# Kernel optimization log

Hardware: AMD Instinct MI355X
Metric: run time of the kernel (lower is better)

## Reference

```python
import jax, jax.numpy as jnp
import numpy as np

VOCAB, EMB, HID, T, B = 10000, 1500, 1500, 35, 64
FORGET_BIAS = 1.0

def setup_inputs() -> dict:
    key = jax.random.key(0)
    ks = jax.random.split(key, 8)
    s = 0.02
    return {
        'x': jax.random.randint(ks[0], (T, B), 0, VOCAB),
        'y': jax.random.randint(ks[1], (T, B), 0, VOCAB),
        'embedding': jax.random.normal(ks[2], (VOCAB, EMB), jnp.float32) * s,
        'W0': jax.random.normal(ks[3], (EMB + HID, 4 * HID), jnp.float32) * s,
        'b0': jnp.zeros((4 * HID,), jnp.float32),
        'W1': jax.random.normal(ks[4], (2 * HID, 4 * HID), jnp.float32) * s,
        'b1': jnp.zeros((4 * HID,), jnp.float32),
        'softmax_w': jax.random.normal(ks[5], (HID, VOCAB), jnp.float32) * 0.1,
        'softmax_b': jnp.zeros((VOCAB,), jnp.float32),
    }

def _lstm_step(c, h, x, W, b):
    # TF LSTMCell: z = [x, h] @ W + b; gate order i, j, f, o; forget_bias added to f
    z = jnp.concatenate([x, h], axis=-1) @ W + b
    i, j, f, o = jnp.split(z, 4, axis=-1)
    c_new = c * jax.nn.sigmoid(f + FORGET_BIAS) + jax.nn.sigmoid(i) * jnp.tanh(j)
    h_new = jnp.tanh(c_new) * jax.nn.sigmoid(o)
    return c_new, h_new

def reference(x, y, embedding, W0, b0, W1, b1, softmax_w, softmax_b):
    inputs = embedding[x]  # [T, B, EMB] (time_major)
    zeros = jnp.zeros((B, HID), inputs.dtype)
    init = (zeros, zeros, zeros, zeros)  # (c0, h0, c1, h1)

    def step(carry, xt):
        c0, h0, c1, h1 = carry
        c0, h0 = _lstm_step(c0, h0, xt, W0, b0)
        c1, h1 = _lstm_step(c1, h1, h0, W1, b1)
        return (c0, h0, c1, h1), h1

    _, outputs = jax.lax.scan(step, init, inputs)  # [T, B, HID]
    logits = outputs.reshape(-1, HID) @ softmax_w + softmax_b  # [T*B, VOCAB]
    logp = jax.nn.log_softmax(logits, axis=-1)
    tgt = y.reshape(-1)
    nll = -jnp.take_along_axis(logp, tgt[:, None], axis=-1)[:, 0]
    loss = jnp.sum(nll) / B  # sequence_loss_by_example with unit weights, / batch_size
    return loss
```

## Files before the change

kernel.cpp:

```cpp
#include <hip/hip_runtime.h>
#include <math.h>

#define TT 35
#define BB 64
#define EMB 1500
#define HID 1500
#define VOCAB 10000
#define KT 3072
#define KG 768
#define NCH 24
#define KLP 1504
#define NBLK 158
#define MROWS 2240
#define MPAD 2304
#define LBLK 94
#define FORGET_BIAS 1.0f

typedef __bf16 bf16x8 __attribute__((ext_vector_type(8)));
typedef float f32x4 __attribute__((ext_vector_type(4)));

__device__ __forceinline__ unsigned short f2bf(float f) {
    unsigned int u = __builtin_bit_cast(unsigned int, f);
    u += 0x7fffu + ((u >> 16) & 1u);
    return (unsigned short)(u >> 16);
}
__device__ __forceinline__ float sigmoidf_(float x) { return 1.0f / (1.0f + expf(-x)); }

#define GLOAD_LDS16(gp, lp) __builtin_amdgcn_global_load_lds( \
    (const __attribute__((address_space(1))) void*)(gp),      \
    (__attribute__((address_space(3))) void*)(lp), 16, 0, 0)

__global__ __launch_bounds__(256) void convT(const float* __restrict__ W,
                                             unsigned short* __restrict__ WT,
                                             int K, int N, int KP) {
    __shared__ float tile[32][33];
    int tx = threadIdx.x, ty = threadIdx.y;
    int n0 = blockIdx.x * 32, k0 = blockIdx.y * 32;
#pragma unroll
    for (int i = 0; i < 4; ++i) {
        int k = k0 + ty + 8 * i, n = n0 + tx;
        tile[ty + 8 * i][tx] = (k < K && n < N) ? W[(size_t)k * N + n] : 0.f;
    }
    __syncthreads();
#pragma unroll
    for (int i = 0; i < 4; ++i) {
        int n = n0 + ty + 8 * i, k = k0 + tx;
        if (n < N) WT[(size_t)n * KP + k] = f2bf(tile[tx][ty + 8 * i]);
    }
}

__global__ __launch_bounds__(256) void embed_kernel(const int* __restrict__ x,
                                                    const float* __restrict__ emb,
                                                    unsigned short* __restrict__ A0) {
    int tok = blockIdx.x;
    int v = x[tok];
    const float* src = emb + (size_t)v * EMB;
    unsigned short* dst = A0 + (size_t)tok * KT;
    for (int i = threadIdx.x; i < EMB; i += 256) dst[i] = f2bf(src[i]);
}

__global__ __launch_bounds__(1024) void lstm_pair(
        const unsigned short* __restrict__ A_0, const unsigned short* __restrict__ WT_0,
        const float* __restrict__ bias_0, float* __restrict__ cst_0,
        unsigned short* __restrict__ d1_0, int s1_0, unsigned short* __restrict__ d2_0, int s2_0,
        const unsigned short* __restrict__ A_1, const unsigned short* __restrict__ WT_1,
        const float* __restrict__ bias_1, float* __restrict__ cst_1,
        unsigned short* __restrict__ d1_1, int s1_1, unsigned short* __restrict__ d2_1, int s2_1) {
    __shared__ __align__(16) unsigned char smem[131072];

    const unsigned short* A;  const unsigned short* WT;
    const float* bias;        float* cst;
    unsigned short* d1; int s1; unsigned short* d2; int s2;
    int nb;
    if (blockIdx.x < LBLK) {
        if (!A_0) return;
        A = A_0; WT = WT_0; bias = bias_0; cst = cst_0;
        d1 = d1_0; s1 = s1_0; d2 = d2_0; s2 = s2_0;
        nb = blockIdx.x;
    } else {
        if (!A_1) return;
        A = A_1; WT = WT_1; bias = bias_1; cst = cst_1;
        d1 = d1_1; s1 = s1_1; d2 = d2_1; s2 = s2_1;
        nb = blockIdx.x - LBLK;
    }

    int tid = threadIdx.x;
    int wv = tid >> 6, lane = tid & 63;
    int mt = wv & 3, kg = wv >> 2;
    int quad = lane >> 4, l16 = lane & 15;
    int col = nb * 16 + l16;

    int rr = lane >> 2, p = lane & 3;
    int sp = p ^ (rr & 3);
    int kbase = kg * KG;
    int q0 = mt * 2, q1 = q0 + 1;
    const unsigned short* gp[2];
    int ldsoff[2];
#pragma unroll
    for (int ii = 0; ii < 2; ++ii) {
        int q = ii ? q1 : q0;
        if (q < 4) {
            gp[ii] = A + (size_t)(16 * q + rr) * KT + kbase + sp * 8;
        } else {
            int g = q - 4;
            int ci = nb * 16 + rr; if (ci > HID - 1) ci = HID - 1;
            gp[ii] = WT + (size_t)(g * HID + ci) * KT + kbase + sp * 8;
        }
        ldsoff[ii] = ((q >> 2) * 4 + kg) * 4096 + (q & 3) * 1024;
    }

    int swz = (quad ^ (l16 & 3)) * 16;
    int aoff = (0 * 4 + kg) * 4096 + (mt * 16 + l16) * 64 + swz;
    int boff = (1 * 4 + kg) * 4096 + l16 * 64 + swz;

    f32x4 acc0 = {0.f,0.f,0.f,0.f}, acc1 = acc0, acc2 = acc0, acc3 = acc0;

#pragma unroll
    for (int ci = 0; ci < 3; ++ci) {
        GLOAD_LDS16(gp[0] + ci * 32, smem + ci * 32768 + ldsoff[0]);
        GLOAD_LDS16(gp[1] + ci * 32, smem + ci * 32768 + ldsoff[1]);
    }

    for (int c = 0; c < NCH; ++c) {
        asm volatile("s_waitcnt vmcnt(4)" ::: "memory");
        __builtin_amdgcn_sched_barrier(0);
        __builtin_amdgcn_s_barrier();
        int cs = (c + 3 < NCH) ? (c + 3) : (NCH - 1);
        int bs_ = (c + 3) & 3;
        GLOAD_LDS16(gp[0] + cs * 32, smem + bs_ * 32768 + ldsoff[0]);
        GLOAD_LDS16(gp[1] + cs * 32, smem + bs_ * 32768 + ldsoff[1]);
        const unsigned char* base = smem + (c & 3) * 32768;
        bf16x8 a  = *(const bf16x8*)(base + aoff);
        bf16x8 b0 = *(const bf16x8*)(base + boff);
        bf16x8 b1 = *(const bf16x8*)(base + boff + 1024);
        bf16x8 b2 = *(const bf16x8*)(base + boff + 2048);
        bf16x8 b3 = *(const bf16x8*)(base + boff + 3072);
        __builtin_amdgcn_s_setprio(1);
        acc0 = __builtin_amdgcn_mfma_f32_16x16x32_bf16(a, b0, acc0, 0, 0, 0);
        acc1 = __builtin_amdgcn_mfma_f32_16x16x32_bf16(a, b1, acc1, 0, 0, 0);
        acc2 = __builtin_amdgcn_mfma_f32_16x16x32_bf16(a, b2, acc2, 0, 0, 0);
        acc3 = __builtin_amdgcn_mfma_f32_16x16x32_bf16(a, b3, acc3, 0, 0, 0);
        __builtin_amdgcn_s_setprio(0);
    }
    asm volatile("s_waitcnt vmcnt(0)" ::: "memory");
    __builtin_amdgcn_sched_barrier(0);
    __syncthreads();

    float* red = (float*)smem;
    if (kg > 0) {
        int w = (kg - 1) * 4 + mt;
#pragma unroll
        for (int r = 0; r < 4; ++r) {
            red[(w * 64 + lane) * 16 + r]      = acc0[r];
            red[(w * 64 + lane) * 16 + 4 + r]  = acc1[r];
            red[(w * 64 + lane) * 16 + 8 + r]  = acc2[r];
            red[(w * 64 + lane) * 16 + 12 + r] = acc3[r];
        }
    }
    __syncthreads();
    if (kg == 0) {
#pragma unroll
        for (int k2 = 0; k2 < 3; ++k2) {
            int w = k2 * 4 + mt;
#pragma unroll
            for (int r = 0; r < 4; ++r) {
                acc0[r] += red[(w * 64 + lane) * 16 + r];
                acc1[r] += red[(w * 64 + lane) * 16 + 4 + r];
                acc2[r] += red[(w * 64 + lane) * 16 + 8 + r];
                acc3[r] += red[(w * 64 + lane) * 16 + 12 + r];
            }
        }
        if (col < HID) {
            float bi = bias[col], bj = bias[HID + col];
            float bf_ = bias[2 * HID + col], bo = bias[3 * HID + col];
#pragma unroll
            for (int r = 0; r < 4; ++r) {
                int row = mt * 16 + quad * 4 + r;
                float zi = acc0[r] + bi;
                float zj = acc1[r] + bj;
                float zf = acc2[r] + bf_;
                float zo = acc3[r] + bo;
                int ci = row * HID + col;
                float cn = cst[ci] * sigmoidf_(zf + FORGET_BIAS) + sigmoidf_(zi) * tanhf(zj);
                float hn = tanhf(cn) * sigmoidf_(zo);
                cst[ci] = cn;
                unsigned short hb = f2bf(hn);
                d1[(size_t)row * s1 + col] = hb;
                if (d2) d2[(size_t)row * s2 + col] = hb;
            }
        }
    }
}

__global__ __launch_bounds__(256) void logits_fold(const unsigned short* __restrict__ A,
                                                   const unsigned short* __restrict__ WT,
                                                   const float* __restrict__ sb,
                                                   const int* __restrict__ y,
                                                   float2* __restrict__ partials,
                                                   float* __restrict__ tgtlog) {
    __shared__ __align__(16) unsigned char smem[32768];

    const int NWG = 79 * 18;
    const int NX = 8;
    const int q = NWG / NX, r = NWG % NX;
    int orig = blockIdx.x + 79 * blockIdx.y;
    int xcd = orig % NX, idx = orig / NX;
    int wgid = (xcd < r ? xcd * (q + 1) : r * (q + 1) + (xcd - r) * q) + idx;
    int bn = wgid % 79, mb = wgid / 79;
    int n0 = bn * 128;

    int tid = threadIdx.x;
    int wv = tid >> 6, lane = tid & 63;
    int wr = wv >> 1, wc = wv & 1;
    int quad = lane >> 4, l16 = lane & 15;

    int rr = lane >> 2;
    int ks = (lane & 3) ^ (rr & 3);
    const unsigned short* gA[2]; const unsigned short* gB[2];
    int ldsA[2], ldsB[2];
#pragma unroll
    for (int i = 0; i < 2; ++i) {
        int r16 = wv * 2 + i;
        int ra = mb * 128 + r16 * 16 + rr;
        gA[i] = A + (size_t)ra * KLP + ks * 8;
        ldsA[i] = r16 * 1024;
        int rb = n0 + r16 * 16 + rr;
        if (rb > VOCAB - 1) rb = VOCAB - 1;
        gB[i] = WT + (size_t)rb * KLP + ks * 8;
        ldsB[i] = 8192 + r16 * 1024;
    }

    int sw16 = (quad ^ (l16 & 3)) * 16;
    int aoff[4], boff[4];
#pragma unroll
    for (int f = 0; f < 4; ++f) {
        aoff[f] = (wr * 64 + f * 16 + l16) * 64 + sw16;
        boff[f] = 8192 + (wc * 64 + f * 16 + l16) * 64 + sw16;
    }

    f32x4 acc[4][4];
#pragma unroll
    for (int i = 0; i < 4; ++i)
#pragma unroll
        for (int j = 0; j < 4; ++j) acc[i][j] = (f32x4){0.f, 0.f, 0.f, 0.f};

#pragma unroll
    for (int i = 0; i < 2; ++i) {
        GLOAD_LDS16(gA[i], smem + ldsA[i]);
        GLOAD_LDS16(gB[i], smem + ldsB[i]);
    }
    __syncthreads();

    for (int c = 0; c < KLP / 32; ++c) {
        int buf = c & 1;
        if (c + 1 < KLP / 32) {
            int ob = (buf ^ 1) * 16384;
#pragma unroll
            for (int i = 0; i < 2; ++i) {
                GLOAD_LDS16(gA[i] + (c + 1) * 32, smem + ob + ldsA[i]);
                GLOAD_LDS16(gB[i] + (c + 1) * 32, smem + ob + ldsB[i]);
            }
        }
        const unsigned char* base = smem + buf * 16384;
        bf16x8 a[4], b[4];
#pragma unroll
        for (int f = 0; f < 4; ++f) {
            a[f] = *(const bf16x8*)(base + aoff[f]);
            b[f] = *(const bf16x8*)(base + boff[f]);
        }
#pragma unroll
        for (int ar = 0; ar < 4; ++ar)
#pragma unroll
            for (int cb = 0; cb < 4; ++cb)
                acc[ar][cb] = __builtin_amdgcn_mfma_f32_16x16x32_bf16(a[ar], b[cb], acc[ar][cb], 0, 0, 0);
        __syncthreads();
    }

    int colv[4]; float bs[4];
#pragma unroll
    for (int cb = 0; cb < 4; ++cb) {
        int c = n0 + wc * 64 + cb * 16 + l16;
        colv[cb] = c;
        int cc = (c < VOCAB) ? c : (VOCAB - 1);
        bs[cb] = sb[cc];
    }
    int nb2 = bn * 2 + wc;
#pragma unroll
    for (int ar = 0; ar < 4; ++ar) {
#pragma unroll
        for (int r2 = 0; r2 < 4; ++r2) {
            float v0 = acc[ar][0][r2] + bs[0];
            float v1 = acc[ar][1][r2] + bs[1];
            float v2 = acc[ar][2][r2] + bs[2];
            float v3 = acc[ar][3][r2] + bs[3];
            if (colv[0] >= VOCAB) v0 = -1e30f;
            if (colv[1] >= VOCAB) v1 = -1e30f;
            if (colv[2] >= VOCAB) v2 = -1e30f;
            if (colv[3] >= VOCAB) v3 = -1e30f;
            int row = mb * 128 + wr * 64 + ar * 16 + quad * 4 + r2;
            int t = y[row < MROWS ? row : 0];
            float tv = -1e30f;
            if (colv[0] == t) tv = v0;
            if (colv[1] == t) tv = v1;
            if (colv[2] == t) tv = v2;
            if (colv[3] == t) tv = v3;
            float mx = fmaxf(fmaxf(v0, v1), fmaxf(v2, v3));
#pragma unroll
            for (int d = 1; d < 16; d <<= 1) mx = fmaxf(mx, __shfl_xor(mx, d, 64));
            float sum = expf(v0 - mx) + expf(v1 - mx) + expf(v2 - mx) + expf(v3 - mx);
#pragma unroll
            for (int d = 1; d < 16; d <<= 1) sum += __shfl_xor(sum, d, 64);
#pragma unroll
            for (int d = 1; d < 16; d <<= 1) tv = fmaxf(tv, __shfl_xor(tv, d, 64));
            if (l16 == 0 && row < MROWS) {
                partials[(size_t)row * NBLK + nb2] = make_float2(mx, sum);
                if (tv > -5e29f) tgtlog[row] = tv;
            }
        }
    }
}

__global__ __launch_bounds__(64) void nll_reduce(const float2* __restrict__ partials,
                                                 const float* __restrict__ tgtlog,
                                                 float* __restrict__ nll) {
    int row = blockIdx.x;
    int lane = threadIdx.x;
    float2 loc[3];
    int cnt = 0;
    float m = -1e30f;
    for (int i = lane; i < NBLK; i += 64) {
        float2 p = partials[(size_t)row * NBLK + i];
        loc[cnt++] = p;
        m = fmaxf(m, p.x);
    }
#pragma unroll
    for (int d = 1; d < 64; d <<= 1) m = fmaxf(m, __shfl_xor(m, d, 64));
    float s = 0.f;
    for (int j = 0; j < cnt; ++j) s += loc[j].y * expf(loc[j].x - m);
#pragma unroll
    for (int d = 1; d < 64; d <<= 1) s += __shfl_xor(s, d, 64);
    if (lane == 0) nll[row] = -(tgtlog[row] - m - logf(s));
}

__global__ __launch_bounds__(256) void loss_kernel(const float* __restrict__ nll,
                                                   float* __restrict__ out) {
    __shared__ float red[256];
    int tid = threadIdx.x;
    float s = 0.f;
    for (int i = tid; i < TT * BB; i += 256) s += nll[i];
    red[tid] = s; __syncthreads();
    for (int st = 128; st > 0; st >>= 1) { if (tid < st) red[tid] += red[tid + st]; __syncthreads(); }
    if (tid == 0) out[0] = red[0] / (float)BB;
}

extern "C" void kernel_launch(void* const* d_in, const int* in_sizes, int n_in,
                              void* d_out, int out_size, void* d_ws, size_t ws_size,
                              hipStream_t stream) {
    const int*   x   = (const int*)d_in[0];
    const int*   y   = (const int*)d_in[1];
    const float* emb = (const float*)d_in[2];
    const float* W0  = (const float*)d_in[3];
    const float* b0  = (const float*)d_in[4];
    const float* W1  = (const float*)d_in[5];
    const float* b1  = (const float*)d_in[6];
    const float* sw  = (const float*)d_in[7];
    const float* sb  = (const float*)d_in[8];
    float* out = (float*)d_out;

    char* p = (char*)d_ws;
    unsigned short* A0   = (unsigned short*)p; p += (size_t)TT * BB * KT * 2;
    unsigned short* A1   = (unsigned short*)p; p += (size_t)2 * BB * KT * 2;
    unsigned short* outs = (unsigned short*)p; p += (size_t)MPAD * KLP * 2;
    float* c0 = (float*)p; p += (size_t)BB * HID * 4;
    float* c1 = (float*)p; p += (size_t)BB * HID * 4;
    size_t zero_bytes = (size_t)(p - (char*)d_ws);
    unsigned short* WbT0 = (unsigned short*)p; p += (size_t)6000 * KT * 2;
    unsigned short* WbT1 = (unsigned short*)p; p += (size_t)6000 * KT * 2;
    unsigned short* swT  = (unsigned short*)p; p += (size_t)VOCAB * KLP * 2;
    float2* partials = (float2*)p; p += (size_t)TT * BB * NBLK * 8;
    float* tgtlog = (float*)p; p += (size_t)TT * BB * 4;
    float* nll    = (float*)p;

    hipMemsetAsync(d_ws, 0, zero_bytes, stream);

    dim3 cblk(32, 8);
    convT<<<dim3(188, 96), cblk, 0, stream>>>(W0, WbT0, 3000, 6000, KT);
    convT<<<dim3(188, 96), cblk, 0, stream>>>(W1, WbT1, 3000, 6000, KT);
    convT<<<dim3(313, 47), cblk, 0, stream>>>(sw, swT, HID, VOCAB, KLP);

    embed_kernel<<<TT * BB, 256, 0, stream>>>(x, emb, A0);

    for (int k = 0; k <= TT; ++k) {
        const unsigned short* A0t = (k < TT) ? A0 + (size_t)k * BB * KT : nullptr;
        unsigned short* d1_0 = A1 + (size_t)(k & 1) * BB * KT;
        unsigned short* d2_0 = (k < TT - 1) ? (A0 + (size_t)(k + 1) * BB * KT + EMB) : nullptr;

        const unsigned short* A1t = (k >= 1) ? A1 + (size_t)((k - 1) & 1) * BB * KT : nullptr;
        unsigned short* d1_1 = A1 + (size_t)(k & 1) * BB * KT + HID;
        unsigned short* d2_1 = (k >= 1) ? outs + (size_t)(k - 1) * BB * KLP : nullptr;

        lstm_pair<<<188, 1024, 0, stream>>>(A0t, WbT0, b0, c0, d1_0, KT, d2_0, KT,
                                            A1t, WbT1, b1, c1, d1_1, KT, d2_1, KLP);
    }

    logits_fold<<<dim3(79, 18), 256, 0, stream>>>(outs, swT, sb, y, partials, tgtlog);
    nll_reduce<<<TT * BB, 64, 0, stream>>>(partials, tgtlog, nll);
    loss_kernel<<<1, 256, 0, stream>>>(nll, out);
}
```

Measured before the change: 1.255 ms.

## Hoist layer-0 input projection out of recurrence into one batched GEMM

Splits W0 into input and hidden halves and precomputes the embedding-times-Wx projection for all timesteps in a single large GEMM (zx_gemm) before the recurrent loop. Each layer-0 step then does only the hidden K=1536 reduction and adds the precomputed bf16 Zx in the epilogue, halving the sequential layer-0 work. This adds an extra kernel, a Zx buffer round trip, and extra bf16 rounding of the input projection. The logits_fold block-to-XCD remapping is also changed to a 1D grid with an explicit assignment.

```diff
diff --git a/kernel.cpp b/kernel.cpp
--- a/kernel.cpp
+++ b/kernel.cpp
@@ -9,11 +9,15 @@
 #define KT 3072
 #define KG 768
 #define NCH 24
+#define KH 1536
+#define KGH 384
+#define NCHH 12
 #define KLP 1504
 #define NBLK 158
 #define MROWS 2240
 #define MPAD 2304
 #define LBLK 94
+#define ZXN 6000
 #define FORGET_BIAS 1.0f
 
 typedef __bf16 bf16x8 __attribute__((ext_vector_type(8)));
@@ -23,6 +27,10 @@
     unsigned int u = __builtin_bit_cast(unsigned int, f);
     u += 0x7fffu + ((u >> 16) & 1u);
     return (unsigned short)(u >> 16);
+}
+__device__ __forceinline__ float bf2f(unsigned short u) {
+    unsigned int v = ((unsigned int)u) << 16;
+    return __builtin_bit_cast(float, v);
 }
 __device__ __forceinline__ float sigmoidf_(float x) { return 1.0f / (1.0f + expf(-x)); }
 
@@ -51,18 +59,104 @@
 
 __global__ __launch_bounds__(256) void embed_kernel(const int* __restrict__ x,
                                                     const float* __restrict__ emb,
-                                                    unsigned short* __restrict__ A0) {
+                                                    unsigned short* __restrict__ Ae) {
     int tok = blockIdx.x;
     int v = x[tok];
     const float* src = emb + (size_t)v * EMB;
-    unsigned short* dst = A0 + (size_t)tok * KT;
+    unsigned short* dst = Ae + (size_t)tok * KH;
     for (int i = threadIdx.x; i < EMB; i += 256) dst[i] = f2bf(src[i]);
+}
+
+__global__ __launch_bounds__(256) void zx_gemm(const unsigned short* __restrict__ A,
+                                               const unsigned short* __restrict__ WT,
+                                               unsigned short* __restrict__ Zx) {
+    __shared__ __align__(16) unsigned char smem[32768];
+    int orig = blockIdx.x;
+    int xcd = orig & 7, j = orig >> 3;
+    int mb, bn;
+    if (xcd < 7) { bn = xcd * 6 + j % 6; mb = j / 6; }
+    else { if (j >= 90) return; bn = 42 + j % 5; mb = j / 5; }
+    int n0 = bn * 128;
+
+    int tid = threadIdx.x;
+    int wv = tid >> 6, lane = tid & 63;
+    int wr = wv >> 1, wc = wv & 1;
+    int quad = lane >> 4, l16 = lane & 15;
+    int rr = lane >> 2;
+    int ks = (lane & 3) ^ (rr & 3);
+    const unsigned short* gA[2]; const unsigned short* gB[2];
+    int ldsA[2], ldsB[2];
+#pragma unroll
+    for (int i = 0; i < 2; ++i) {
+        int r16 = wv * 2 + i;
+        int ra = mb * 128 + r16 * 16 + rr;
+        gA[i] = A + (size_t)ra * KH + ks * 8;
+        ldsA[i] = r16 * 1024;
+        int rb = n0 + r16 * 16 + rr;
+        if (rb > 5999) rb = 5999;
+        gB[i] = WT + (size_t)rb * KH + ks * 8;
+        ldsB[i] = 8192 + r16 * 1024;
+    }
+    int sw16 = (quad ^ (l16 & 3)) * 16;
+    int aoff[4], boff[4];
+#pragma unroll
+    for (int f = 0; f < 4; ++f) {
+        aoff[f] = (wr * 64 + f * 16 + l16) * 64 + sw16;
+        boff[f] = 8192 + (wc * 64 + f * 16 + l16) * 64 + sw16;
+    }
+    f32x4 acc[4][4];
+#pragma unroll
+    for (int i = 0; i < 4; ++i)
+#pragma unroll
+        for (int jj = 0; jj < 4; ++jj) acc[i][jj] = (f32x4){0.f, 0.f, 0.f, 0.f};
+
+#pragma unroll
+    for (int i = 0; i < 2; ++i) {
+        GLOAD_LDS16(gA[i], smem + ldsA[i]);
+        GLOAD_LDS16(gB[i], smem + ldsB[i]);
+    }
+    __syncthreads();
+    for (int c = 0; c < KH / 32; ++c) {
+        int buf = c & 1;
+        if (c + 1 < KH / 32) {
+            int ob = (buf ^ 1) * 16384;
+#pragma unroll
+            for (int i = 0; i < 2; ++i) {
+                GLOAD_LDS16(gA[i] + (c + 1) * 32, smem + ob + ldsA[i]);
+                GLOAD_LDS16(gB[i] + (c + 1) * 32, smem + ob + ldsB[i]);
+            }
+        }
+        const unsigned char* base = smem + buf * 16384;
+        bf16x8 a[4], b[4];
+#pragma unroll
+        for (int f = 0; f < 4; ++f) {
+            a[f] = *(const bf16x8*)(base + aoff[f]);
+            b[f] = *(const bf16x8*)(base + boff[f]);
+        }
+#pragma unroll
+        for (int ar = 0; ar < 4; ++ar)
+#pragma unroll
+            for (int cb = 0; cb < 4; ++cb)
+                acc[ar][cb] = __builtin_amdgcn_mfma_f32_16x16x32_bf16(a[ar], b[cb], acc[ar][cb], 0, 0, 0);
+        __syncthreads();
+    }
+#pragma unroll
+    for (int ar = 0; ar < 4; ++ar)
+#pragma unroll
+        for (int cb = 0; cb < 4; ++cb)
+#pragma unroll
+            for (int r2 = 0; r2 < 4; ++r2) {
+                int row = mb * 128 + wr * 64 + ar * 16 + quad * 4 + r2;
+                int col = n0 + wc * 64 + cb * 16 + l16;
+                if (col < ZXN) Zx[(size_t)row * ZXN + col] = f2bf(acc[ar][cb][r2]);
+            }
 }
 
 __global__ __launch_bounds__(1024) void lstm_pair(
         const unsigned short* __restrict__ A_0, const unsigned short* __restrict__ WT_0,
         const float* __restrict__ bias_0, float* __restrict__ cst_0,
         unsigned short* __restrict__ d1_0, int s1_0, unsigned short* __restrict__ d2_0, int s2_0,
+        const unsigned short* __restrict__ zx_0,
         const unsigned short* __restrict__ A_1, const unsigned short* __restrict__ WT_1,
         const float* __restrict__ bias_1, float* __restrict__ cst_1,
         unsigned short* __restrict__ d1_1, int s1_1, unsigned short* __restrict__ d2_1, int s2_1) {
@@ -71,16 +165,19 @@
     const unsigned short* A;  const unsigned short* WT;
     const float* bias;        float* cst;
     unsigned short* d1; int s1; unsigned short* d2; int s2;
-    int nb;
+    const unsigned short* zx;
+    int nb, kstr, kgK, nch;
     if (blockIdx.x < LBLK) {
         if (!A_0) return;
         A = A_0; WT = WT_0; bias = bias_0; cst = cst_0;
         d1 = d1_0; s1 = s1_0; d2 = d2_0; s2 = s2_0;
+        zx = zx_0; kstr = KH; kgK = KGH; nch = NCHH;
         nb = blockIdx.x;
     } else {
         if (!A_1) return;
         A = A_1; WT = WT_1; bias = bias_1; cst = cst_1;
         d1 = d1_1; s1 = s1_1; d2 = d2_1; s2 = s2_1;
+        zx = nullptr; kstr = KT; kgK = KG; nch = NCH;
         nb = blockIdx.x - LBLK;
     }
 
@@ -92,7 +189,7 @@
 
     int rr = lane >> 2, p = lane & 3;
     int sp = p ^ (rr & 3);
-    int kbase = kg * KG;
+    int kbase = kg * kgK;
     int q0 = mt * 2, q1 = q0 + 1;
     const unsigned short* gp[2];
     int ldsoff[2];
@@ -100,11 +197,11 @@
     for (int ii = 0; ii < 2; ++ii) {
         int q = ii ? q1 : q0;
         if (q < 4) {
-            gp[ii] = A + (size_t)(16 * q + rr) * KT + kbase + sp * 8;
+            gp[ii] = A + (size_t)(16 * q + rr) * kstr + kbase + sp * 8;
         } else {
             int g = q - 4;
             int ci = nb * 16 + rr; if (ci > HID - 1) ci = HID - 1;
-            gp[ii] = WT + (size_t)(g * HID + ci) * KT + kbase + sp * 8;
+            gp[ii] = WT + (size_t)(g * HID + ci) * kstr + kbase + sp * 8;
         }
         ldsoff[ii] = ((q >> 2) * 4 + kg) * 4096 + (q & 3) * 1024;
     }
@@ -121,11 +218,11 @@
         GLOAD_LDS16(gp[1] + ci * 32, smem + ci * 32768 + ldsoff[1]);
     }
 
-    for (int c = 0; c < NCH; ++c) {
+    for (int c = 0; c < nch; ++c) {
         asm volatile("s_waitcnt vmcnt(4)" ::: "memory");
         __builtin_amdgcn_sched_barrier(0);
         __builtin_amdgcn_s_barrier();
-        int cs = (c + 3 < NCH) ? (c + 3) : (NCH - 1);
+        int cs = (c + 3 < nch) ? (c + 3) : (nch - 1);
         int bs_ = (c + 3) & 3;
         GLOAD_LDS16(gp[0] + cs * 32, smem + bs_ * 32768 + ldsoff[0]);
         GLOAD_LDS16(gp[1] + cs * 32, smem + bs_ * 32768 + ldsoff[1]);
@@ -180,6 +277,13 @@
                 float zj = acc1[r] + bj;
                 float zf = acc2[r] + bf_;
                 float zo = acc3[r] + bo;
+                if (zx) {
+                    const unsigned short* zr = zx + (size_t)row * ZXN;
+                    zi += bf2f(zr[col]);
+                    zj += bf2f(zr[HID + col]);
+                    zf += bf2f(zr[2 * HID + col]);
+                    zo += bf2f(zr[3 * HID + col]);
+                }
                 int ci = row * HID + col;
                 float cn = cst[ci] * sigmoidf_(zf + FORGET_BIAS) + sigmoidf_(zi) * tanhf(zj);
                 float hn = tanhf(cn) * sigmoidf_(zo);
@@ -200,13 +304,11 @@
                                                    float* __restrict__ tgtlog) {
     __shared__ __align__(16) unsigned char smem[32768];
 
-    const int NWG = 79 * 18;
-    const int NX = 8;
-    const int q = NWG / NX, r = NWG % NX;
-    int orig = blockIdx.x + 79 * blockIdx.y;
-    int xcd = orig % NX, idx = orig / NX;
-    int wgid = (xcd < r ? xcd * (q + 1) : r * (q + 1) + (xcd - r) * q) + idx;
-    int bn = wgid % 79, mb = wgid / 79;
+    int orig = blockIdx.x;
+    int xcd = orig & 7, j = orig >> 3;
+    int mb, bn;
+    if (xcd < 7) { bn = xcd * 10 + j % 10; mb = j / 10; }
+    else { if (j >= 162) return; bn = 70 + j % 9; mb = j / 9; }
     int n0 = bn * 128;
 
     int tid = threadIdx.x;
@@ -242,7 +344,7 @@
 #pragma unroll
     for (int i = 0; i < 4; ++i)
 #pragma unroll
-        for (int j = 0; j < 4; ++j) acc[i][j] = (f32x4){0.f, 0.f, 0.f, 0.f};
+        for (int jj = 0; jj < 4; ++jj) acc[i][jj] = (f32x4){0.f, 0.f, 0.f, 0.f};
 
 #pragma unroll
     for (int i = 0; i < 2; ++i) {
@@ -336,7 +438,7 @@
 #pragma unroll
     for (int d = 1; d < 64; d <<= 1) m = fmaxf(m, __shfl_xor(m, d, 64));
     float s = 0.f;
-    for (int j = 0; j < cnt; ++j) s += loc[j].y * expf(loc[j].x - m);
+    for (int jj = 0; jj < cnt; ++jj) s += loc[jj].y * expf(loc[jj].x - m);
 #pragma unroll
     for (int d = 1; d < 64; d <<= 1) s += __shfl_xor(s, d, 64);
     if (lane == 0) nll[row] = -(tgtlog[row] - m - logf(s));
@@ -368,13 +470,16 @@
     float* out = (float*)d_out;
 
     char* p = (char*)d_ws;
-    unsigned short* A0   = (unsigned short*)p; p += (size_t)TT * BB * KT * 2;
+    unsigned short* Ae   = (unsigned short*)p; p += (size_t)MPAD * KH * 2;
     unsigned short* A1   = (unsigned short*)p; p += (size_t)2 * BB * KT * 2;
+    unsigned short* H0   = (unsigned short*)p; p += (size_t)2 * BB * KH * 2;
     unsigned short* outs = (unsigned short*)p; p += (size_t)MPAD * KLP * 2;
     float* c0 = (float*)p; p += (size_t)BB * HID * 4;
     float* c1 = (float*)p; p += (size_t)BB * HID * 4;
     size_t zero_bytes = (size_t)(p - (char*)d_ws);
-    unsigned short* WbT0 = (unsigned short*)p; p += (size_t)6000 * KT * 2;
+    unsigned short* Zx   = (unsigned short*)p; p += (size_t)MPAD * ZXN * 2;
+    unsigned short* WxT0 = (unsigned short*)p; p += (size_t)6000 * KH * 2;
+    unsigned short* WhT0 = (unsigned short*)p; p += (size_t)6000 * KH * 2;
     unsigned short* WbT1 = (unsigned short*)p; p += (size_t)6000 * KT * 2;
     unsigned short* swT  = (unsigned short*)p; p += (size_t)VOCAB * KLP * 2;
     float2* partials = (float2*)p; p += (size_t)TT * BB * NBLK * 8;
@@ -384,26 +489,29 @@
     hipMemsetAsync(d_ws, 0, zero_bytes, stream);
 
     dim3 cblk(32, 8);
-    convT<<<dim3(188, 96), cblk, 0, stream>>>(W0, WbT0, 3000, 6000, KT);
+    convT<<<dim3(188, 48), cblk, 0, stream>>>(W0, WxT0, 1500, 6000, KH);
+    convT<<<dim3(188, 48), cblk, 0, stream>>>(W0 + (size_t)1500 * 6000, WhT0, 1500, 6000, KH);
     convT<<<dim3(188, 96), cblk, 0, stream>>>(W1, WbT1, 3000, 6000, KT);
     convT<<<dim3(313, 47), cblk, 0, stream>>>(sw, swT, HID, VOCAB, KLP);
 
-    embed_kernel<<<TT * BB, 256, 0, stream>>>(x, emb, A0);
+    embed_kernel<<<TT * BB, 256, 0, stream>>>(x, emb, Ae);
+    zx_gemm<<<864, 256, 0, stream>>>(Ae, WxT0, Zx);
 
     for (int k = 0; k <= TT; ++k) {
-        const unsigned short* A0t = (k < TT) ? A0 + (size_t)k * BB * KT : nullptr;
+        const unsigned short* A0t = (k < TT) ? H0 + (size_t)((k - 1) & 1) * BB * KH : nullptr;
         unsigned short* d1_0 = A1 + (size_t)(k & 1) * BB * KT;
-        unsigned short* d2_0 = (k < TT - 1) ? (A0 + (size_t)(k + 1) * BB * KT + EMB) : nullptr;
+        unsigned short* d2_0 = H0 + (size_t)(k & 1) * BB * KH;
+        const unsigned short* zx0 = Zx + (size_t)k * BB * ZXN;
 
         const unsigned short* A1t = (k >= 1) ? A1 + (size_t)((k - 1) & 1) * BB * KT : nullptr;
         unsigned short* d1_1 = A1 + (size_t)(k & 1) * BB * KT + HID;
         unsigned short* d2_1 = (k >= 1) ? outs + (size_t)(k - 1) * BB * KLP : nullptr;
 
-        lstm_pair<<<188, 1024, 0, stream>>>(A0t, WbT0, b0, c0, d1_0, KT, d2_0, KT,
+        lstm_pair<<<188, 1024, 0, stream>>>(A0t, WhT0, b0, c0, d1_0, KT, d2_0, KH, zx0,
                                             A1t, WbT1, b1, c1, d1_1, KT, d2_1, KLP);
     }
 
-    logits_fold<<<dim3(79, 18), 256, 0, stream>>>(outs, swT, sb, y, partials, tgtlog);
+    logits_fold<<<1440, 256, 0, stream>>>(outs, swT, sb, y, partials, tgtlog);
     nll_reduce<<<TT * BB, 64, 0, stream>>>(partials, tgtlog, nll);
     loss_kernel<<<1, 256, 0, stream>>>(nll, out);
 }
```

After: 1.303 ms. 3.9% more time.

## Deepen logits GEMM pipeline, remap blocks per XCD, strengthen LDS swizzle

Applied to the files above, without the earlier changes.

The logits GEMM moves from a double-buffered to a 4-stage LDS ring with loads issued three chunks ahead. It uses a waitcnt plus a raw barrier in place of the two syncthreads per iteration, and raises wave priority around the MFMA block. Workgroups are remapped so each XCD owns a contiguous band of vocabulary columns, which is meant to improve L2 reuse of the softmax weights. Both the LSTM and logits kernels get an extra XOR term in the LDS swizzle to cut bank conflicts. The cost is 64KB of LDS per block, which may lower occupancy, and a 1D launch with early-exit blocks on the last XCD.

```diff
diff --git a/kernel.cpp b/kernel.cpp
--- a/kernel.cpp
+++ b/kernel.cpp
@@ -91,7 +91,7 @@
     int col = nb * 16 + l16;
 
     int rr = lane >> 2, p = lane & 3;
-    int sp = p ^ (rr & 3);
+    int sp = p ^ (rr & 3) ^ ((rr >> 2) & 3);
     int kbase = kg * KG;
     int q0 = mt * 2, q1 = q0 + 1;
     const unsigned short* gp[2];
@@ -109,7 +109,7 @@
         ldsoff[ii] = ((q >> 2) * 4 + kg) * 4096 + (q & 3) * 1024;
     }
 
-    int swz = (quad ^ (l16 & 3)) * 16;
+    int swz = (quad ^ (l16 & 3) ^ ((l16 >> 2) & 3)) * 16;
     int aoff = (0 * 4 + kg) * 4096 + (mt * 16 + l16) * 64 + swz;
     int boff = (1 * 4 + kg) * 4096 + l16 * 64 + swz;
 
@@ -198,15 +198,13 @@
                                                    const int* __restrict__ y,
                                                    float2* __restrict__ partials,
                                                    float* __restrict__ tgtlog) {
-    __shared__ __align__(16) unsigned char smem[32768];
-
-    const int NWG = 79 * 18;
-    const int NX = 8;
-    const int q = NWG / NX, r = NWG % NX;
-    int orig = blockIdx.x + 79 * blockIdx.y;
-    int xcd = orig % NX, idx = orig / NX;
-    int wgid = (xcd < r ? xcd * (q + 1) : r * (q + 1) + (xcd - r) * q) + idx;
-    int bn = wgid % 79, mb = wgid / 79;
+    __shared__ __align__(16) unsigned char smem[65536];
+
+    int orig = blockIdx.x;
+    int xcd = orig & 7, j = orig >> 3;
+    int mb, bn;
+    if (xcd < 7) { bn = xcd * 10 + j % 10; mb = j / 10; }
+    else { if (j >= 162) return; bn = 70 + j % 9; mb = j / 9; }
     int n0 = bn * 128;
 
     int tid = threadIdx.x;
@@ -215,7 +213,7 @@
     int quad = lane >> 4, l16 = lane & 15;
 
     int rr = lane >> 2;
-    int ks = (lane & 3) ^ (rr & 3);
+    int ks = (lane & 3) ^ (rr & 3) ^ ((rr >> 2) & 3);
     const unsigned short* gA[2]; const unsigned short* gB[2];
     int ldsA[2], ldsB[2];
 #pragma unroll
@@ -230,7 +228,7 @@
         ldsB[i] = 8192 + r16 * 1024;
     }
 
-    int sw16 = (quad ^ (l16 & 3)) * 16;
+    int sw16 = (quad ^ (l16 & 3) ^ ((l16 >> 2) & 3)) * 16;
     int aoff[4], boff[4];
 #pragma unroll
     for (int f = 0; f < 4; ++f) {
@@ -242,47 +240,53 @@
 #pragma unroll
     for (int i = 0; i < 4; ++i)
 #pragma unroll
-        for (int j = 0; j < 4; ++j) acc[i][j] = (f32x4){0.f, 0.f, 0.f, 0.f};
-
-#pragma unroll
-    for (int i = 0; i < 2; ++i) {
-        GLOAD_LDS16(gA[i], smem + ldsA[i]);
-        GLOAD_LDS16(gB[i], smem + ldsB[i]);
-    }
-    __syncthreads();
-
-    for (int c = 0; c < KLP / 32; ++c) {
-        int buf = c & 1;
-        if (c + 1 < KLP / 32) {
-            int ob = (buf ^ 1) * 16384;
-#pragma unroll
-            for (int i = 0; i < 2; ++i) {
-                GLOAD_LDS16(gA[i] + (c + 1) * 32, smem + ob + ldsA[i]);
-                GLOAD_LDS16(gB[i] + (c + 1) * 32, smem + ob + ldsB[i]);
-            }
-        }
-        const unsigned char* base = smem + buf * 16384;
+        for (int jj = 0; jj < 4; ++jj) acc[i][jj] = (f32x4){0.f, 0.f, 0.f, 0.f};
+
+    const int NCHL = KLP / 32;
+#pragma unroll
+    for (int ci = 0; ci < 3; ++ci)
+#pragma unroll
+        for (int i = 0; i < 2; ++i) {
+            GLOAD_LDS16(gA[i] + ci * 32, smem + ci * 16384 + ldsA[i]);
+            GLOAD_LDS16(gB[i] + ci * 32, smem + ci * 16384 + ldsB[i]);
+        }
+    for (int c = 0; c < NCHL; ++c) {
+        asm volatile("s_waitcnt vmcnt(8)" ::: "memory");
+        __builtin_amdgcn_sched_barrier(0);
+        __builtin_amdgcn_s_barrier();
+        int cs = (c + 3 < NCHL) ? (c + 3) : (NCHL - 1);
+        int ob = ((c + 3) & 3) * 16384;
+#pragma unroll
+        for (int i = 0; i < 2; ++i) {
+            GLOAD_LDS16(gA[i] + cs * 32, smem + ob + ldsA[i]);
+            GLOAD_LDS16(gB[i] + cs * 32, smem + ob + ldsB[i]);
+        }
+        const unsigned char* base = smem + (c & 3) * 16384;
         bf16x8 a[4], b[4];
 #pragma unroll
         for (int f = 0; f < 4; ++f) {
             a[f] = *(const bf16x8*)(base + aoff[f]);
             b[f] = *(const bf16x8*)(base + boff[f]);
         }
+        __builtin_amdgcn_s_setprio(1);
 #pragma unroll
         for (int ar = 0; ar < 4; ++ar)
 #pragma unroll
-            for (int cb = 0; cb < 4; ++cb)
-                acc[ar][cb] = __builtin_amdgcn_mfma_f32_16x16x32_bf16(a[ar], b[cb], acc[ar][cb], 0, 0, 0);
-        __syncthreads();
-    }
+            for (int cbv = 0; cbv < 4; ++cbv)
+                acc[ar][cbv] = __builtin_amdgcn_mfma_f32_16x16x32_bf16(a[ar], b[cbv], acc[ar][cbv], 0, 0, 0);
+        __builtin_amdgcn_s_setprio(0);
+    }
+    asm volatile("s_waitcnt vmcnt(0)" ::: "memory");
+    __builtin_amdgcn_sched_barrier(0);
+    __syncthreads();
 
     int colv[4]; float bs[4];
 #pragma unroll
-    for (int cb = 0; cb < 4; ++cb) {
-        int c = n0 + wc * 64 + cb * 16 + l16;
-        colv[cb] = c;
+    for (int cbv = 0; cbv < 4; ++cbv) {
+        int c = n0 + wc * 64 + cbv * 16 + l16;
+        colv[cbv] = c;
         int cc = (c < VOCAB) ? c : (VOCAB - 1);
-        bs[cb] = sb[cc];
+        bs[cbv] = sb[cc];
     }
     int nb2 = bn * 2 + wc;
 #pragma unroll
@@ -336,7 +340,7 @@
 #pragma unroll
     for (int d = 1; d < 64; d <<= 1) m = fmaxf(m, __shfl_xor(m, d, 64));
     float s = 0.f;
-    for (int j = 0; j < cnt; ++j) s += loc[j].y * expf(loc[j].x - m);
+    for (int jj = 0; jj < cnt; ++jj) s += loc[jj].y * expf(loc[jj].x - m);
 #pragma unroll
     for (int d = 1; d < 64; d <<= 1) s += __shfl_xor(s, d, 64);
     if (lane == 0) nll[row] = -(tgtlog[row] - m - logf(s));
@@ -403,7 +407,7 @@
                                             A1t, WbT1, b1, c1, d1_1, KT, d2_1, KLP);
     }
 
-    logits_fold<<<dim3(79, 18), 256, 0, stream>>>(outs, swT, sb, y, partials, tgtlog);
+    logits_fold<<<1440, 256, 0, stream>>>(outs, swT, sb, y, partials, tgtlog);
     nll_reduce<<<TT * BB, 64, 0, stream>>>(partials, tgtlog, nll);
     loss_kernel<<<1, 256, 0, stream>>>(nll, out);
 }
```

New measurement: 1.261 ms. No clear change (+0.5%).

## Overlap logits tiles with LSTM recurrence and strengthen LDS swizzle

Applied to the files above, without the earlier changes.

Each recurrent lstm_pair launch now carries up to 48 extra blocks that compute logits/softmax tiles for output rows already produced, which fills idle CUs during the latency-bound recurrence. The remaining tiles run in a reduced logits_fold launch afterward. The LSTM LDS swizzle also gains an extra XOR term to cut bank conflicts. Trade-offs: the extra blocks reserve 128KB of LDS while using only 256 of 1024 threads, and they may contend with the critical-path LSTM blocks. The logits_fold XCD-aware tile remapping is also dropped.

```diff
diff --git a/kernel.cpp b/kernel.cpp
--- a/kernel.cpp
+++ b/kernel.cpp
@@ -14,6 +14,7 @@
 #define MROWS 2240
 #define MPAD 2304
 #define LBLK 94
+#define NTILE 1422
 #define FORGET_BIAS 1.0f
 
 typedef __bf16 bf16x8 __attribute__((ext_vector_type(8)));
@@ -59,14 +60,142 @@
     for (int i = threadIdx.x; i < EMB; i += 256) dst[i] = f2bf(src[i]);
 }
 
+__device__ __forceinline__ void logits_tile_body(
+        int tile, const unsigned short* __restrict__ A,
+        const unsigned short* __restrict__ WT,
+        const float* __restrict__ sb, const int* __restrict__ y,
+        float2* __restrict__ partials, float* __restrict__ tgtlog,
+        unsigned char* smem, int tid) {
+    int mb = tile / 79, bn = tile % 79;
+    int n0 = bn * 128;
+    int wv = tid >> 6, lane = tid & 63;
+    int wr = wv >> 1, wc = wv & 1;
+    int quad = lane >> 4, l16 = lane & 15;
+
+    int rr = lane >> 2;
+    int ks = (lane & 3) ^ (rr & 3);
+    const unsigned short* gA[2]; const unsigned short* gB[2];
+    int ldsA[2], ldsB[2];
+#pragma unroll
+    for (int i = 0; i < 2; ++i) {
+        int r16 = wv * 2 + i;
+        int ra = mb * 128 + r16 * 16 + rr;
+        gA[i] = A + (size_t)ra * KLP + ks * 8;
+        ldsA[i] = r16 * 1024;
+        int rb = n0 + r16 * 16 + rr;
+        if (rb > VOCAB - 1) rb = VOCAB - 1;
+        gB[i] = WT + (size_t)rb * KLP + ks * 8;
+        ldsB[i] = 8192 + r16 * 1024;
+    }
+
+    int sw16 = (quad ^ (l16 & 3)) * 16;
+    int aoff[4], boff[4];
+#pragma unroll
+    for (int f = 0; f < 4; ++f) {
+        aoff[f] = (wr * 64 + f * 16 + l16) * 64 + sw16;
+        boff[f] = 8192 + (wc * 64 + f * 16 + l16) * 64 + sw16;
+    }
+
+    f32x4 acc[4][4];
+#pragma unroll
+    for (int i = 0; i < 4; ++i)
+#pragma unroll
+        for (int jj = 0; jj < 4; ++jj) acc[i][jj] = (f32x4){0.f, 0.f, 0.f, 0.f};
+
+#pragma unroll
+    for (int i = 0; i < 2; ++i) {
+        GLOAD_LDS16(gA[i], smem + ldsA[i]);
+        GLOAD_LDS16(gB[i], smem + ldsB[i]);
+    }
+    __syncthreads();
+
+    for (int c = 0; c < KLP / 32; ++c) {
+        int buf = c & 1;
+        if (c + 1 < KLP / 32) {
+            int ob = (buf ^ 1) * 16384;
+#pragma unroll
+            for (int i = 0; i < 2; ++i) {
+                GLOAD_LDS16(gA[i] + (c + 1) * 32, smem + ob + ldsA[i]);
+                GLOAD_LDS16(gB[i] + (c + 1) * 32, smem + ob + ldsB[i]);
+            }
+        }
+        const unsigned char* base = smem + buf * 16384;
+        bf16x8 a[4], b[4];
+#pragma unroll
+        for (int f = 0; f < 4; ++f) {
+            a[f] = *(const bf16x8*)(base + aoff[f]);
+            b[f] = *(const bf16x8*)(base + boff[f]);
+        }
+#pragma unroll
+        for (int ar = 0; ar < 4; ++ar)
+#pragma unroll
+            for (int cbv = 0; cbv < 4; ++cbv)
+                acc[ar][cbv] = __builtin_amdgcn_mfma_f32_16x16x32_bf16(a[ar], b[cbv], acc[ar][cbv], 0, 0, 0);
+        __syncthreads();
+    }
+
+    int colv[4]; float bs[4];
+#pragma unroll
+    for (int cbv = 0; cbv < 4; ++cbv) {
+        int c = n0 + wc * 64 + cbv * 16 + l16;
+        colv[cbv] = c;
+        int cc = (c < VOCAB) ? c : (VOCAB - 1);
+        bs[cbv] = sb[cc];
+    }
+    int nb2 = bn * 2 + wc;
+#pragma unroll
+    for (int ar = 0; ar < 4; ++ar) {
+#pragma unroll
+        for (int r2 = 0; r2 < 4; ++r2) {
+            float v0 = acc[ar][0][r2] + bs[0];
+            float v1 = acc[ar][1][r2] + bs[1];
+            float v2 = acc[ar][2][r2] + bs[2];
+            float v3 = acc[ar][3][r2] + bs[3];
+            if (colv[0] >= VOCAB) v0 = -1e30f;
+            if (colv[1] >= VOCAB) v1 = -1e30f;
+            if (colv[2] >= VOCAB) v2 = -1e30f;
+            if (colv[3] >= VOCAB) v3 = -1e30f;
+            int row = mb * 128 + wr * 64 + ar * 16 + quad * 4 + r2;
+            int t = y[row < MROWS ? row : 0];
+            float tv = -1e30f;
+            if (colv[0] == t) tv = v0;
+            if (colv[1] == t) tv = v1;
+            if (colv[2] == t) tv = v2;
+            if (colv[3] == t) tv = v3;
+            float mx = fmaxf(fmaxf(v0, v1), fmaxf(v2, v3));
+#pragma unroll
+            for (int d = 1; d < 16; d <<= 1) mx = fmaxf(mx, __shfl_xor(mx, d, 64));
+            float sum = expf(v0 - mx) + expf(v1 - mx) + expf(v2 - mx) + expf(v3 - mx);
+#pragma unroll
+            for (int d = 1; d < 16; d <<= 1) sum += __shfl_xor(sum, d, 64);
+#pragma unroll
+            for (int d = 1; d < 16; d <<= 1) tv = fmaxf(tv, __shfl_xor(tv, d, 64));
+            if (l16 == 0 && row < MROWS) {
+                partials[(size_t)row * NBLK + nb2] = make_float2(mx, sum);
+                if (tv > -5e29f) tgtlog[row] = tv;
+            }
+        }
+    }
+}
+
 __global__ __launch_bounds__(1024) void lstm_pair(
         const unsigned short* __restrict__ A_0, const unsigned short* __restrict__ WT_0,
         const float* __restrict__ bias_0, float* __restrict__ cst_0,
         unsigned short* __restrict__ d1_0, int s1_0, unsigned short* __restrict__ d2_0, int s2_0,
         const unsigned short* __restrict__ A_1, const unsigned short* __restrict__ WT_1,
         const float* __restrict__ bias_1, float* __restrict__ cst_1,
-        unsigned short* __restrict__ d1_1, int s1_1, unsigned short* __restrict__ d2_1, int s2_1) {
+        unsigned short* __restrict__ d1_1, int s1_1, unsigned short* __restrict__ d2_1, int s2_1,
+        const unsigned short* __restrict__ outsA, const unsigned short* __restrict__ swT,
+        const float* __restrict__ sb, const int* __restrict__ y,
+        float2* __restrict__ partials, float* __restrict__ tgtlog, int tile0) {
     __shared__ __align__(16) unsigned char smem[131072];
+
+    if (blockIdx.x >= 2 * LBLK) {
+        if (threadIdx.x >= 256) return;
+        logits_tile_body(tile0 + (int)blockIdx.x - 2 * LBLK, outsA, swT, sb, y,
+                         partials, tgtlog, smem, (int)threadIdx.x);
+        return;
+    }
 
     const unsigned short* A;  const unsigned short* WT;
     const float* bias;        float* cst;
@@ -91,7 +220,7 @@
     int col = nb * 16 + l16;
 
     int rr = lane >> 2, p = lane & 3;
-    int sp = p ^ (rr & 3);
+    int sp = p ^ (rr & 3) ^ ((rr >> 2) & 3);
     int kbase = kg * KG;
     int q0 = mt * 2, q1 = q0 + 1;
     const unsigned short* gp[2];
@@ -109,7 +238,7 @@
         ldsoff[ii] = ((q >> 2) * 4 + kg) * 4096 + (q & 3) * 1024;
     }
 
-    int swz = (quad ^ (l16 & 3)) * 16;
+    int swz = (quad ^ (l16 & 3) ^ ((l16 >> 2) & 3)) * 16;
     int aoff = (0 * 4 + kg) * 4096 + (mt * 16 + l16) * 64 + swz;
     int boff = (1 * 4 + kg) * 4096 + l16 * 64 + swz;
 
@@ -197,127 +326,10 @@
                                                    const float* __restrict__ sb,
                                                    const int* __restrict__ y,
                                                    float2* __restrict__ partials,
-                                                   float* __restrict__ tgtlog) {
+                                                   float* __restrict__ tgtlog, int tile0) {
     __shared__ __align__(16) unsigned char smem[32768];
-
-    const int NWG = 79 * 18;
-    const int NX = 8;
-    const int q = NWG / NX, r = NWG % NX;
-    int orig = blockIdx.x + 79 * blockIdx.y;
-    int xcd = orig % NX, idx = orig / NX;
-    int wgid = (xcd < r ? xcd * (q + 1) : r * (q + 1) + (xcd - r) * q) + idx;
-    int bn = wgid % 79, mb = wgid / 79;
-    int n0 = bn * 128;
-
-    int tid = threadIdx.x;
-    int wv = tid >> 6, lane = tid & 63;
-    int wr = wv >> 1, wc = wv & 1;
-    int quad = lane >> 4, l16 = lane & 15;
-
-    int rr = lane >> 2;
-    int ks = (lane & 3) ^ (rr & 3);
-    const unsigned short* gA[2]; const unsigned short* gB[2];
-    int ldsA[2], ldsB[2];
-#pragma unroll
-    for (int i = 0; i < 2; ++i) {
-        int r16 = wv * 2 + i;
-        int ra = mb * 128 + r16 * 16 + rr;
-        gA[i] = A + (size_t)ra * KLP + ks * 8;
-        ldsA[i] = r16 * 1024;
-        int rb = n0 + r16 * 16 + rr;
-        if (rb > VOCAB - 1) rb = VOCAB - 1;
-        gB[i] = WT + (size_t)rb * KLP + ks * 8;
-        ldsB[i] = 8192 + r16 * 1024;
-    }
-
-    int sw16 = (quad ^ (l16 & 3)) * 16;
-    int aoff[4], boff[4];
-#pragma unroll
-    for (int f = 0; f < 4; ++f) {
-        aoff[f] = (wr * 64 + f * 16 + l16) * 64 + sw16;
-        boff[f] = 8192 + (wc * 64 + f * 16 + l16) * 64 + sw16;
-    }
-
-    f32x4 acc[4][4];
-#pragma unroll
-    for (int i = 0; i < 4; ++i)
-#pragma unroll
-        for (int j = 0; j < 4; ++j) acc[i][j] = (f32x4){0.f, 0.f, 0.f, 0.f};
-
-#pragma unroll
-    for (int i = 0; i < 2; ++i) {
-        GLOAD_LDS16(gA[i], smem + ldsA[i]);
-        GLOAD_LDS16(gB[i], smem + ldsB[i]);
-    }
-    __syncthreads();
-
-    for (int c = 0; c < KLP / 32; ++c) {
-        int buf = c & 1;
-        if (c + 1 < KLP / 32) {
-            int ob = (buf ^ 1) * 16384;
-#pragma unroll
-            for (int i = 0; i < 2; ++i) {
-                GLOAD_LDS16(gA[i] + (c + 1) * 32, smem + ob + ldsA[i]);
-                GLOAD_LDS16(gB[i] + (c + 1) * 32, smem + ob + ldsB[i]);
-            }
-        }
-        const unsigned char* base = smem + buf * 16384;
-        bf16x8 a[4], b[4];
-#pragma unroll
-        for (int f = 0; f < 4; ++f) {
-            a[f] = *(const bf16x8*)(base + aoff[f]);
-            b[f] = *(const bf16x8*)(base + boff[f]);
-        }
-#pragma unroll
-        for (int ar = 0; ar < 4; ++ar)
-#pragma unroll
-            for (int cb = 0; cb < 4; ++cb)
-                acc[ar][cb] = __builtin_amdgcn_mfma_f32_16x16x32_bf16(a[ar], b[cb], acc[ar][cb], 0, 0, 0);
-        __syncthreads();
-    }
-
-    int colv[4]; float bs[4];
-#pragma unroll
-    for (int cb = 0; cb < 4; ++cb) {
-        int c = n0 + wc * 64 + cb * 16 + l16;
-        colv[cb] = c;
-        int cc = (c < VOCAB) ? c : (VOCAB - 1);
-        bs[cb] = sb[cc];
-    }
-    int nb2 = bn * 2 + wc;
-#pragma unroll
-    for (int ar = 0; ar < 4; ++ar) {
-#pragma unroll
-        for (int r2 = 0; r2 < 4; ++r2) {
-            float v0 = acc[ar][0][r2] + bs[0];
-            float v1 = acc[ar][1][r2] + bs[1];
-            float v2 = acc[ar][2][r2] + bs[2];
-            float v3 = acc[ar][3][r2] + bs[3];
-            if (colv[0] >= VOCAB) v0 = -1e30f;
-            if (colv[1] >= VOCAB) v1 = -1e30f;
-            if (colv[2] >= VOCAB) v2 = -1e30f;
-            if (colv[3] >= VOCAB) v3 = -1e30f;
-            int row = mb * 128 + wr * 64 + ar * 16 + quad * 4 + r2;
-            int t = y[row < MROWS ? row : 0];
-            float tv = -1e30f;
-            if (colv[0] == t) tv = v0;
-            if (colv[1] == t) tv = v1;
-            if (colv[2] == t) tv = v2;
-            if (colv[3] == t) tv = v3;
-            float mx = fmaxf(fmaxf(v0, v1), fmaxf(v2, v3));
-#pragma unroll
-            for (int d = 1; d < 16; d <<= 1) mx = fmaxf(mx, __shfl_xor(mx, d, 64));
-            float sum = expf(v0 - mx) + expf(v1 - mx) + expf(v2 - mx) + expf(v3 - mx);
-#pragma unroll
-            for (int d = 1; d < 16; d <<= 1) sum += __shfl_xor(sum, d, 64);
-#pragma unroll
-            for (int d = 1; d < 16; d <<= 1) tv = fmaxf(tv, __shfl_xor(tv, d, 64));
-            if (l16 == 0 && row < MROWS) {
-                partials[(size_t)row * NBLK + nb2] = make_float2(mx, sum);
-                if (tv > -5e29f) tgtlog[row] = tv;
-            }
-        }
-    }
+    logits_tile_body(tile0 + (int)blockIdx.x, A, WT, sb, y, partials, tgtlog,
+                     smem, (int)threadIdx.x);
 }
 
 __global__ __launch_bounds__(64) void nll_reduce(const float2* __restrict__ partials,
@@ -336,7 +348,7 @@
 #pragma unroll
     for (int d = 1; d < 64; d <<= 1) m = fmaxf(m, __shfl_xor(m, d, 64));
     float s = 0.f;
-    for (int j = 0; j < cnt; ++j) s += loc[j].y * expf(loc[j].x - m);
+    for (int jj = 0; jj < cnt; ++jj) s += loc[jj].y * expf(loc[jj].x - m);
 #pragma unroll
     for (int d = 1; d < 64; d <<= 1) s += __shfl_xor(s, d, 64);
     if (lane == 0) nll[row] = -(tgtlog[row] - m - logf(s));
@@ -390,6 +402,7 @@
 
     embed_kernel<<<TT * BB, 256, 0, stream>>>(x, emb, A0);
 
+    int S = 0;
     for (int k = 0; k <= TT; ++k) {
         const unsigned short* A0t = (k < TT) ? A0 + (size_t)k * BB * KT : nullptr;
         unsigned short* d1_0 = A1 + (size_t)(k & 1) * BB * KT;
@@ -399,11 +412,19 @@
         unsigned short* d1_1 = A1 + (size_t)(k & 1) * BB * KT + HID;
         unsigned short* d2_1 = (k >= 1) ? outs + (size_t)(k - 1) * BB * KLP : nullptr;
 
-        lstm_pair<<<188, 1024, 0, stream>>>(A0t, WbT0, b0, c0, d1_0, KT, d2_0, KT,
-                                            A1t, WbT1, b1, c1, d1_1, KT, d2_1, KLP);
-    }
-
-    logits_fold<<<dim3(79, 18), 256, 0, stream>>>(outs, swT, sb, y, partials, tgtlog);
+        int avail = 0;
+        if (k >= 3) { int m = (k - 1) / 2; avail = 79 * m; if (avail > NTILE) avail = NTILE; }
+        int cnt = avail - S; if (cnt > 48) cnt = 48; if (cnt < 0) cnt = 0;
+
+        lstm_pair<<<2 * LBLK + cnt, 1024, 0, stream>>>(
+            A0t, WbT0, b0, c0, d1_0, KT, d2_0, KT,
+            A1t, WbT1, b1, c1, d1_1, KT, d2_1, KLP,
+            outs, swT, sb, y, partials, tgtlog, S);
+        S += cnt;
+    }
+
+    if (S < NTILE)
+        logits_fold<<<NTILE - S, 256, 0, stream>>>(outs, swT, sb, y, partials, tgtlog, S);
     nll_reduce<<<TT * BB, 64, 0, stream>>>(partials, tgtlog, nll);
     loss_kernel<<<1, 256, 0, stream>>>(nll, out);
 }
```

After: 1.792 ms. 42.8% more time.
